# Performance work log

Hardware: AMD Instinct MI355X
Metric: run time of the kernel (lower is better)

The kernel has to match this reference:

```python
import jax, jax.numpy as jnp
import numpy as np

GAMMA = 1.0

def setup_inputs() -> dict:
    key = jax.random.key(0)
    kx, ky = jax.random.split(key)
    x = jax.random.normal(kx, (8192, 256), dtype=jnp.float32)
    y = jax.random.normal(ky, (8192, 256), dtype=jnp.float32)
    return {"x": x, "y": y}

def reference(x, y):
    # RBF kernel K[i,j] = exp(-gamma * ||x_i - y_j||^2)
    # materializing the O(N*M*D) broadcast difference tensor.
    x2 = jnp.sum(x * x, axis=-1)            # [N]
    y2 = jnp.sum(y * y, axis=-1)            # [M]
    xy = jnp.einsum('nd,md->nm', x, y)      # [N, M] GEMM
    dist2 = x2[:, None] + y2[None, :] - 2.0 * xy
    dist2 = jnp.maximum(dist2, 0.0)         # guard tiny negative round-off
    return jnp.exp(-GAMMA * dist2)
```

## Files before the change

### kernel.cpp

```cpp
#include <hip/hip_runtime.h>


#define M_DIM 8192
#define K_DIM 256
#define BM 128
#define BN 128
#define BK 64

typedef __attribute__((ext_vector_type(8))) short short8;
typedef __attribute__((ext_vector_type(4))) float float4v;

__device__ inline unsigned short f2bf(float f) {
    union { float f; unsigned int u; } a; a.f = f;
    unsigned int u = a.u;
    unsigned int r = u + 0x7fffu + ((u >> 16) & 1u);
    return (unsigned short)(r >> 16);
}

__global__ __launch_bounds__(256) void prep_kernel(
        const float* __restrict__ x, const float* __restrict__ y,
        unsigned short* __restrict__ xb, unsigned short* __restrict__ yb,
        float* __restrict__ x2, float* __restrict__ y2) {
    int row  = blockIdx.x * 4 + (threadIdx.x >> 6);
    int lane = threadIdx.x & 63;

    const float* src; unsigned short* dst; float* nrm; int r;
    if (row < M_DIM) { src = x; dst = xb; nrm = x2; r = row; }
    else             { src = y; dst = yb; nrm = y2; r = row - M_DIM; }

    const float4* s4 = (const float4*)(src + (size_t)r * K_DIM);
    float4 v = s4[lane];
    float ss = v.x * v.x + v.y * v.y + v.z * v.z + v.w * v.w;

    ushort4 p;
    p.x = f2bf(v.x); p.y = f2bf(v.y); p.z = f2bf(v.z); p.w = f2bf(v.w);
    ((ushort4*)(dst + (size_t)r * K_DIM))[lane] = p;

    #pragma unroll
    for (int o = 32; o > 0; o >>= 1) ss += __shfl_down(ss, o);
    if (lane == 0) nrm[r] = ss;
}

__global__ __launch_bounds__(256, 2) void rbf_gemm(
        const unsigned short* __restrict__ xb, const unsigned short* __restrict__ yb,
        const float* __restrict__ x2, const float* __restrict__ y2,
        float* __restrict__ out) {
    __shared__ __align__(16) unsigned short As[BM * BK];
    __shared__ __align__(16) unsigned short Bs[BN * BK];

    const int tid  = threadIdx.x;
    const int wid  = tid >> 6;
    const int lane = tid & 63;
    const int wm   = wid >> 1;
    const int wn   = wid & 1;
    const int m0   = blockIdx.y * BM;
    const int n0   = blockIdx.x * BN;

    float4v acc[4][4] = {};

    const int lrow8 = lane >> 3;
    const int lchk  = lane & 7;

    for (int kt = 0; kt < K_DIM; kt += BK) {
        #pragma unroll
        for (int i = 0; i < 4; ++i) {
            int rbase = i * 32 + wid * 8;
            const unsigned short* ga = xb
                + (size_t)(m0 + rbase + lrow8) * K_DIM + kt + lchk * 8;
            __builtin_amdgcn_global_load_lds(
                (__attribute__((address_space(1))) void*)ga,
                (__attribute__((address_space(3))) void*)&As[rbase * BK],
                16, 0, 0);
        }
        #pragma unroll
        for (int i = 0; i < 4; ++i) {
            int rbase = i * 32 + wid * 8;
            const unsigned short* gb = yb
                + (size_t)(n0 + rbase + lrow8) * K_DIM + kt + lchk * 8;
            __builtin_amdgcn_global_load_lds(
                (__attribute__((address_space(1))) void*)gb,
                (__attribute__((address_space(3))) void*)&Bs[rbase * BK],
                16, 0, 0);
        }
        __syncthreads();

        #pragma unroll
        for (int ks = 0; ks < 2; ++ks) {
            const int colk = ks * 32 + (lane >> 4) * 8;
            short8 af[4], bfr[4];
            #pragma unroll
            for (int mt = 0; mt < 4; ++mt)
                af[mt] = *(const short8*)&As[(wm * 64 + mt * 16 + (lane & 15)) * BK + colk];
            #pragma unroll
            for (int nt = 0; nt < 4; ++nt)
                bfr[nt] = *(const short8*)&Bs[(wn * 64 + nt * 16 + (lane & 15)) * BK + colk];
            #pragma unroll
            for (int mt = 0; mt < 4; ++mt)
                #pragma unroll
                for (int nt = 0; nt < 4; ++nt)
                    acc[mt][nt] = __builtin_amdgcn_mfma_f32_16x16x32_bf16(
                        af[mt], bfr[nt], acc[mt][nt], 0, 0, 0);
        }
        __syncthreads();
    }

    const int q = lane >> 4;
    const int c = lane & 15;
    #pragma unroll
    for (int mt = 0; mt < 4; ++mt) {
        const int rowb = m0 + wm * 64 + mt * 16 + q * 4;
        float x2v[4];
        #pragma unroll
        for (int v = 0; v < 4; ++v) x2v[v] = x2[rowb + v];
        #pragma unroll
        for (int nt = 0; nt < 4; ++nt) {
            const int col = n0 + wn * 64 + nt * 16 + c;
            const float y2v = y2[col];
            #pragma unroll
            for (int v = 0; v < 4; ++v) {
                float d = x2v[v] + y2v - 2.0f * acc[mt][nt][v];
                d = fmaxf(d, 0.0f);
                out[(size_t)(rowb + v) * M_DIM + col] = __expf(-d);
            }
        }
    }
}

__global__ void rbf_naive(const float* __restrict__ x, const float* __restrict__ y,
                          float* __restrict__ out) {
    __shared__ float xs[16][17];
    __shared__ float ys[16][17];
    const int tx = threadIdx.x, ty = threadIdx.y;
    const int row = blockIdx.y * 16 + ty;
    const int col = blockIdx.x * 16 + tx;
    float acc = 0.0f;
    for (int k0 = 0; k0 < K_DIM; k0 += 16) {
        xs[ty][tx] = x[(size_t)row * K_DIM + k0 + tx];
        ys[ty][tx] = y[(size_t)(blockIdx.x * 16 + ty) * K_DIM + k0 + tx];
        __syncthreads();
        #pragma unroll
        for (int kk = 0; kk < 16; ++kk) {
            float d = xs[ty][kk] - ys[tx][kk];
            acc += d * d;
        }
        __syncthreads();
    }
    out[(size_t)row * M_DIM + col] = __expf(-acc);
}

extern "C" void kernel_launch(void* const* d_in, const int* in_sizes, int n_in,
                              void* d_out, int out_size, void* d_ws, size_t ws_size,
                              hipStream_t stream) {
    const float* x = (const float*)d_in[0];
    const float* y = (const float*)d_in[1];
    float* out = (float*)d_out;

    const size_t need = (size_t)2 * M_DIM * K_DIM * sizeof(unsigned short)
                      + (size_t)2 * M_DIM * sizeof(float);
    if (ws_size >= need) {
        unsigned short* xb = (unsigned short*)d_ws;
        unsigned short* yb = xb + (size_t)M_DIM * K_DIM;
        float* x2 = (float*)(yb + (size_t)M_DIM * K_DIM);
        float* y2 = x2 + M_DIM;

        prep_kernel<<<dim3((2 * M_DIM) / 4), dim3(256), 0, stream>>>(x, y, xb, yb, x2, y2);
        rbf_gemm<<<dim3(M_DIM / BN, M_DIM / BM), dim3(256), 0, stream>>>(xb, yb, x2, y2, out);
    } else {
        rbf_naive<<<dim3(M_DIM / 16, M_DIM / 16), dim3(16, 16), 0, stream>>>(x, y, out);
    }
}
```

Baseline: 290.3 us.

## Load MFMA fragments directly from global memory with register double-buffering, drop LDS

```diff
diff --git a/kernel.cpp b/kernel.cpp
--- a/kernel.cpp
+++ b/kernel.cpp
@@ -3,9 +3,6 @@
 
 #define M_DIM 8192
 #define K_DIM 256
-#define BM 128
-#define BN 128
-#define BK 64
 
 typedef __attribute__((ext_vector_type(8))) short short8;
 typedef __attribute__((ext_vector_type(4))) float float4v;
@@ -41,80 +38,63 @@
     if (lane == 0) nrm[r] = ss;
 }
 
-__global__ __launch_bounds__(256, 2) void rbf_gemm(
+__global__ __launch_bounds__(256, 3) void rbf_gemm(
         const unsigned short* __restrict__ xb, const unsigned short* __restrict__ yb,
         const float* __restrict__ x2, const float* __restrict__ y2,
         float* __restrict__ out) {
-    __shared__ __align__(16) unsigned short As[BM * BK];
-    __shared__ __align__(16) unsigned short Bs[BN * BK];
-
     const int tid  = threadIdx.x;
     const int wid  = tid >> 6;
     const int lane = tid & 63;
     const int wm   = wid >> 1;
     const int wn   = wid & 1;
-    const int m0   = blockIdx.y * BM;
-    const int n0   = blockIdx.x * BN;
+    const int m0   = blockIdx.y * 128 + wm * 64;
+    const int n0   = blockIdx.x * 128 + wn * 64;
+
+    const int fr = lane & 15;
+    const int kc = (lane >> 4) * 8;
+
+    const unsigned short* pa = xb + (size_t)(m0 + fr) * K_DIM + kc;
+    const unsigned short* pb = yb + (size_t)(n0 + fr) * K_DIM + kc;
 
     float4v acc[4][4] = {};
+    short8 af[2][4], bf[2][4];
 
-    const int lrow8 = lane >> 3;
-    const int lchk  = lane & 7;
+    #pragma unroll
+    for (int t = 0; t < 4; ++t) {
+        af[0][t] = *(const short8*)(pa + (size_t)t * 16 * K_DIM);
+        bf[0][t] = *(const short8*)(pb + (size_t)t * 16 * K_DIM);
+    }
 
-    for (int kt = 0; kt < K_DIM; kt += BK) {
-        #pragma unroll
-        for (int i = 0; i < 4; ++i) {
-            int rbase = i * 32 + wid * 8;
-            const unsigned short* ga = xb
-                + (size_t)(m0 + rbase + lrow8) * K_DIM + kt + lchk * 8;
-            __builtin_amdgcn_global_load_lds(
-                (__attribute__((address_space(1))) void*)ga,
-                (__attribute__((address_space(3))) void*)&As[rbase * BK],
-                16, 0, 0);
+    #pragma unroll
+    for (int k = 0; k < 8; ++k) {
+        const int cur = k & 1, nxt = cur ^ 1;
+        if (k < 7) {
+            const int ko = (k + 1) * 32;
+            #pragma unroll
+            for (int t = 0; t < 4; ++t) {
+                af[nxt][t] = *(const short8*)(pa + (size_t)t * 16 * K_DIM + ko);
+                bf[nxt][t] = *(const short8*)(pb + (size_t)t * 16 * K_DIM + ko);
+            }
         }
         #pragma unroll
-        for (int i = 0; i < 4; ++i) {
-            int rbase = i * 32 + wid * 8;
-            const unsigned short* gb = yb
-                + (size_t)(n0 + rbase + lrow8) * K_DIM + kt + lchk * 8;
-            __builtin_amdgcn_global_load_lds(
-                (__attribute__((address_space(1))) void*)gb,
-                (__attribute__((address_space(3))) void*)&Bs[rbase * BK],
-                16, 0, 0);
-        }
-        __syncthreads();
-
-        #pragma unroll
-        for (int ks = 0; ks < 2; ++ks) {
-            const int colk = ks * 32 + (lane >> 4) * 8;
-            short8 af[4], bfr[4];
-            #pragma unroll
-            for (int mt = 0; mt < 4; ++mt)
-                af[mt] = *(const short8*)&As[(wm * 64 + mt * 16 + (lane & 15)) * BK + colk];
+        for (int mt = 0; mt < 4; ++mt)
             #pragma unroll
             for (int nt = 0; nt < 4; ++nt)
-                bfr[nt] = *(const short8*)&Bs[(wn * 64 + nt * 16 + (lane & 15)) * BK + colk];
-            #pragma unroll
-            for (int mt = 0; mt < 4; ++mt)
-                #pragma unroll
-                for (int nt = 0; nt < 4; ++nt)
-                    acc[mt][nt] = __builtin_amdgcn_mfma_f32_16x16x32_bf16(
-                        af[mt], bfr[nt], acc[mt][nt], 0, 0, 0);
-        }
-        __syncthreads();
+                acc[mt][nt] = __builtin_amdgcn_mfma_f32_16x16x32_bf16(
+                    af[cur][mt], bf[cur][nt], acc[mt][nt], 0, 0, 0);
     }
 
     const int q = lane >> 4;
     const int c = lane & 15;
     #pragma unroll
     for (int mt = 0; mt < 4; ++mt) {
-        const int rowb = m0 + wm * 64 + mt * 16 + q * 4;
+        const int rowb = m0 + mt * 16 + q * 4;
         float x2v[4];
         #pragma unroll
         for (int v = 0; v < 4; ++v) x2v[v] = x2[rowb + v];
         #pragma unroll
         for (int nt = 0; nt < 4; ++nt) {
-            const int col = n0 + wn * 64 + nt * 16 + c;
+            const int col = n0 + nt * 16 + c;
             const float y2v = y2[col];
             #pragma unroll
             for (int v = 0; v < 4; ++v) {
@@ -164,7 +144,7 @@
         float* y2 = x2 + M_DIM;
 
         prep_kernel<<<dim3((2 * M_DIM) / 4), dim3(256), 0, stream>>>(x, y, xb, yb, x2, y2);
-        rbf_gemm<<<dim3(M_DIM / BN, M_DIM / BM), dim3(256), 0, stream>>>(xb, yb, x2, y2, out);
+        rbf_gemm<<<dim3(M_DIM / 128, M_DIM / 128), dim3(256), 0, stream>>>(xb, yb, x2, y2, out);
     } else {
         rbf_naive<<<dim3(M_DIM / 16, M_DIM / 16), dim3(16, 16), 0, stream>>>(x, y, out);
     }
```

Measured after the change: 368.6 us. 1.27x slower.
